# Kernel tuning notes

Measured on AMD Instinct MI355X. Metric: run time of the kernel, lower is better.

The kernel has to match this reference:

```python
import jax, jax.numpy as jnp
import numpy as np

B, T, N_EMBD, HEAD = 8, 2048, 1024, 64

def setup_inputs() -> dict:
    key = jax.random.key(0)
    k1, k2, k3, k4 = jax.random.split(key, 4)
    scale = 0.02
    return {
        "x": jax.random.normal(k1, (B, T, N_EMBD), dtype=jnp.float32),
        "Wk": jax.random.normal(k2, (N_EMBD, HEAD), dtype=jnp.float32) * scale,
        "Wq": jax.random.normal(k3, (N_EMBD, HEAD), dtype=jnp.float32) * scale,
        "Wv": jax.random.normal(k4, (N_EMBD, HEAD), dtype=jnp.float32) * scale,
    }

def reference(x, Wk, Wq, Wv):
    # x: [B, T, C]; projections are bias-free Linear(C -> head_size)
    Bx, Tx, C = x.shape
    k = x @ Wk  # [B, T, H]
    q = x @ Wq  # [B, T, H]
    v = x @ Wv  # [B, T, H]
    # NOTE: original scales by C**-0.5 with C = n_embd (not head_size)
    wei = jnp.einsum('bth,bsh->bts', q, k) * (C ** -0.5)  # [B, T, T]
    causal = jnp.tril(jnp.ones((Tx, Tx), dtype=bool))
    wei = jnp.where(causal, wei, -jnp.inf)
    wei = jax.nn.softmax(wei, axis=-1)
    out = jnp.einsum('bts,bsh->bth', wei, v)  # [B, T, H]
    return out
```

## Files before the change

kernel.cpp:

```cpp
#include <hip/hip_runtime.h>
#include <math.h>

#define B_ 8
#define T_ 2048
#define C_ 1024
#define H_ 64

typedef __attribute__((ext_vector_type(8))) short bf16x8;
typedef __attribute__((ext_vector_type(4))) float f32x4;
typedef __attribute__((ext_vector_type(16))) float f32x16;
typedef __attribute__((ext_vector_type(4))) unsigned u32x4;
typedef __attribute__((ext_vector_type(2))) unsigned u32x2;

static __device__ __forceinline__ short f2bf(float f) {
    unsigned u = __float_as_uint(f);
    unsigned r = (u + 0x7FFFu + ((u >> 16) & 1u)) >> 16;
    return (short)r;
}

static __device__ __forceinline__ unsigned cvt_pk_bf16(float lo, float hi) {
    unsigned r;
    asm("v_cvt_pk_bf16_f32 %0, %1, %2" : "=v"(r) : "v"(lo), "v"(hi));
    return r;
}

static __device__ __forceinline__ u32x2 p32(unsigned a, unsigned b) {
    return __builtin_amdgcn_permlane32_swap(a, b, false, false);
}
static __device__ __forceinline__ float xmax32(float x) {
    u32x2 r = p32(__float_as_uint(x), __float_as_uint(x));
    return fmaxf(__uint_as_float(r[0]), __uint_as_float(r[1]));
}
static __device__ __forceinline__ float xsum32(float x) {
    u32x2 r = p32(__float_as_uint(x), __float_as_uint(x));
    return __uint_as_float(r[0]) + __uint_as_float(r[1]);
}


__global__ __launch_bounds__(256) void wtrans_kernel(
    const float* __restrict__ Wq, const float* __restrict__ Wk,
    const float* __restrict__ Wv, short* __restrict__ WT)
{
    const int n  = blockIdx.x;
    const int k0 = threadIdx.x * 4;
    const float* Wsel = (n < 64) ? Wq : (n < 128 ? Wk : Wv);
    const int h = n & 63;
    short4 pk;
    pk.x = f2bf(Wsel[(size_t)(k0 + 0) * H_ + h]);
    pk.y = f2bf(Wsel[(size_t)(k0 + 1) * H_ + h]);
    pk.z = f2bf(Wsel[(size_t)(k0 + 2) * H_ + h]);
    pk.w = f2bf(Wsel[(size_t)(k0 + 3) * H_ + h]);
    *reinterpret_cast<short4*>(&WT[(size_t)n * C_ + k0]) = pk;
}

__global__ __launch_bounds__(256) void proj_kernel(
    const float* __restrict__ x, const short* __restrict__ WT,
    short* __restrict__ qF, short* __restrict__ kF, short* __restrict__ vF)
{
    __shared__ short Xs[32][72];
    __shared__ short Ws[192][72];

    const int tid  = threadIdx.x;
    const int m0   = blockIdx.x * 32;
    const int w    = tid >> 6;
    const int rs   = w >> 1;
    const int ch   = w & 1;
    const int lane = tid & 63;
    const int col  = lane & 15;
    const int g    = lane >> 4;

    const int srow = tid >> 3;
    const int sk0  = (tid & 7) * 8;
    const float* xs_src = &x[(size_t)(m0 + srow) * C_ + sk0];

    int wrow[6], wc8[6];
#pragma unroll
    for (int t6 = 0; t6 < 6; ++t6) {
        int idx = tid + t6 * 256;
        wrow[t6] = idx >> 3;
        wc8[t6]  = (idx & 7) * 8;
    }

    f32x4 acc[6];
#pragma unroll
    for (int nt = 0; nt < 6; ++nt) acc[nt] = (f32x4){0.f, 0.f, 0.f, 0.f};

    float4 xa0 = *reinterpret_cast<const float4*>(xs_src);
    float4 xb0 = *reinterpret_cast<const float4*>(xs_src + 4);
    float4 xa1 = *reinterpret_cast<const float4*>(xs_src + 64);
    float4 xb1 = *reinterpret_cast<const float4*>(xs_src + 68);
    bf16x8 wr[6];
#pragma unroll
    for (int t6 = 0; t6 < 6; ++t6)
        wr[t6] = *reinterpret_cast<const bf16x8*>(&WT[(size_t)wrow[t6] * C_ + wc8[t6]]);

#define PROJ_STEP(KB, XA, XB)                                                  \
    {                                                                          \
        __syncthreads();                                                       \
        u32x4 xw;                                                              \
        xw[0] = cvt_pk_bf16((XA).x, (XA).y);                                   \
        xw[1] = cvt_pk_bf16((XA).z, (XA).w);                                   \
        xw[2] = cvt_pk_bf16((XB).x, (XB).y);                                   \
        xw[3] = cvt_pk_bf16((XB).z, (XB).w);                                   \
        *reinterpret_cast<u32x4*>(&Xs[srow][sk0]) = xw;                        \
        _Pragma("unroll")                                                      \
        for (int t6 = 0; t6 < 6; ++t6)                                         \
            *reinterpret_cast<bf16x8*>(&Ws[wrow[t6]][wc8[t6]]) = wr[t6];       \
        __syncthreads();                                                       \
        if ((KB) + 128 < C_) {                                                 \
            XA = *reinterpret_cast<const float4*>(xs_src + (KB) + 128);        \
            XB = *reinterpret_cast<const float4*>(xs_src + (KB) + 132);        \
        }                                                                      \
        if ((KB) + 64 < C_) {                                                  \
            _Pragma("unroll")                                                  \
            for (int t6 = 0; t6 < 6; ++t6)                                     \
                wr[t6] = *reinterpret_cast<const bf16x8*>(                     \
                    &WT[(size_t)wrow[t6] * C_ + (KB) + 64 + wc8[t6]]);         \
        }                                                                      \
        bf16x8 a0 = *reinterpret_cast<const bf16x8*>(&Xs[rs * 16 + col][g * 8]);      \
        bf16x8 a1 = *reinterpret_cast<const bf16x8*>(&Xs[rs * 16 + col][32 + g * 8]); \
        _Pragma("unroll")                                                      \
        for (int nt = 0; nt < 6; ++nt) {                                       \
            const int ng = ch * 6 + nt;                                        \
            bf16x8 b0 = *reinterpret_cast<const bf16x8*>(&Ws[ng * 16 + col][g * 8]);      \
            bf16x8 b1 = *reinterpret_cast<const bf16x8*>(&Ws[ng * 16 + col][32 + g * 8]); \
            acc[nt] = __builtin_amdgcn_mfma_f32_16x16x32_bf16(a0, b0, acc[nt], 0, 0, 0);  \
            acc[nt] = __builtin_amdgcn_mfma_f32_16x16x32_bf16(a1, b1, acc[nt], 0, 0, 0);  \
        }                                                                      \
    }

    for (int s2 = 0; s2 < 8; ++s2) {
        const int kb = s2 * 128;
        PROJ_STEP(kb, xa0, xb0);
        PROJ_STEP(kb + 64, xa1, xb1);
    }
#undef PROJ_STEP

    const int trow0 = m0 + rs * 16 + g * 4;
    const int bb    = trow0 >> 11;
    const int tloc  = trow0 & 2047;
    const size_t base = (size_t)bb * T_ * H_;
    const int hiq = col >> 3, eq = col & 7;
#pragma unroll
    for (int nt = 0; nt < 6; ++nt) {
        const int ng = ch * 6 + nt;
        if (ng < 4) {
#pragma unroll
            for (int r = 0; r < 4; ++r) {
                const int tl  = tloc + r;
                const int jq  = tl >> 5, lnq = tl & 31;
                qF[base + (size_t)(((jq * 4 + ng) * 64) + hiq * 32 + lnq) * 8 + eq]
                    = f2bf(acc[nt][r]);
            }
        } else if (ng < 8) {
#pragma unroll
            for (int r = 0; r < 4; ++r) {
                const int tl   = tloc + r;
                const int kb2  = tl >> 6, half = (tl >> 5) & 1, lnk = tl & 31;
                kF[base + (size_t)((((kb2 * 2 + half) * 4 + (ng - 4)) * 64)
                                   + hiq * 32 + lnk) * 8 + eq]
                    = f2bf(acc[nt][r]);
            }
        } else {
            const int kb2 = tloc >> 6, kt = (tloc >> 4) & 3;
            const int vhi = (tloc >> 3) & 1, e0 = tloc & 7;
            const int h   = (ng - 8) * 16 + col;
            const int hs  = h >> 5, vln = h & 31;
            short4 pk;
            pk.x = f2bf(acc[nt][0]); pk.y = f2bf(acc[nt][1]);
            pk.z = f2bf(acc[nt][2]); pk.w = f2bf(acc[nt][3]);
            *reinterpret_cast<short4*>(
                &vF[base + (size_t)((((kb2 * 2 + hs) * 4 + kt) * 64)
                                    + vhi * 32 + vln) * 8 + e0]) = pk;
        }
    }
}

__global__ __launch_bounds__(512) void attn_kernel(
    const short* __restrict__ qF, const short* __restrict__ kF,
    const short* __restrict__ vF, float* __restrict__ out)
{
    __shared__ float Ob[8][32][68];
    __shared__ float Ml[8][32][2];

    const int tid  = threadIdx.x;
    const int w    = tid >> 6;
    const int lane = tid & 63;
    const int ln   = lane & 31;
    const int hi   = lane >> 5;
    const int bid  = blockIdx.x;
    const int b    = bid & 7;
    const int j    = 63 - (bid >> 3);
    const int qt0  = j * 32;
    const int n64  = (j >> 1) + 1;

    const size_t base = (size_t)b * T_ * H_;
    const short* qFb = qF + base;
    const short* kFb = kF + base;
    const short* vFb = vF + base;

    bf16x8 qf[4];
#pragma unroll
    for (int ht = 0; ht < 4; ++ht)
        qf[ht] = *reinterpret_cast<const bf16x8*>(
            &qFb[(size_t)((j * 4 + ht) * 64 + lane) * 8]);

    float m_i = -INFINITY, l_i = 0.f;
    f32x16 acc0, acc1;
#pragma unroll
    for (int r = 0; r < 16; ++r) { acc0[r] = 0.f; acc1[r] = 0.f; }

    for (int kb = w; kb < n64; kb += 8) {
        const short* kblk = &kFb[(size_t)kb * 4096];
        const short* vblk = &vFb[(size_t)kb * 4096];

        f32x16 s0, s1;
#pragma unroll
        for (int r = 0; r < 16; ++r) { s0[r] = 0.f; s1[r] = 0.f; }
#pragma unroll
        for (int ht = 0; ht < 4; ++ht) {
            bf16x8 ka0 = *reinterpret_cast<const bf16x8*>(
                &kblk[(size_t)((ht * 64) + lane) * 8]);
            bf16x8 ka1 = *reinterpret_cast<const bf16x8*>(
                &kblk[(size_t)(((4 + ht) * 64) + lane) * 8]);
            s0 = __builtin_amdgcn_mfma_f32_32x32x16_bf16(ka0, qf[ht], s0, 0, 0, 0);
            s1 = __builtin_amdgcn_mfma_f32_32x32x16_bf16(ka1, qf[ht], s1, 0, 0, 0);
        }

        bf16x8 va0[4];
#pragma unroll
        for (int kt = 0; kt < 4; ++kt)
            va0[kt] = *reinterpret_cast<const bf16x8*>(
                &vblk[(size_t)((kt * 64) + lane) * 8]);

#pragma unroll
        for (int r = 0; r < 16; ++r) { s0[r] *= 0.03125f; s1[r] *= 0.03125f; }
        if (kb == n64 - 1) {
            const int qglob = qt0 + ln;
            const int kb0   = kb * 64 + hi * 4;
#pragma unroll
            for (int r = 0; r < 16; ++r) {
                const int key = kb0 + (r & 3) + 8 * (r >> 2);
                if (key > qglob)      s0[r] = -INFINITY;
                if (key + 32 > qglob) s1[r] = -INFINITY;
            }
        }

        float t8[8];
#pragma unroll
        for (int r = 0; r < 8; ++r)
            t8[r] = fmaxf(fmaxf(s0[r], s0[r + 8]), fmaxf(s1[r], s1[r + 8]));
#pragma unroll
        for (int r = 0; r < 4; ++r) t8[r] = fmaxf(t8[r], t8[r + 4]);
        float mx = fmaxf(fmaxf(t8[0], t8[2]), fmaxf(t8[1], t8[3]));
        mx = xmax32(mx);

        const float mn    = fmaxf(m_i, mx);
        const float alpha = __expf(m_i - mn);
        m_i = mn;

#pragma unroll
        for (int r = 0; r < 16; ++r) {
            s0[r] = __expf(s0[r] - mn);
            s1[r] = __expf(s1[r] - mn);
        }
#pragma unroll
        for (int r = 0; r < 8; ++r)
            t8[r] = (s0[r] + s0[r + 8]) + (s1[r] + s1[r + 8]);
#pragma unroll
        for (int r = 0; r < 4; ++r) t8[r] = t8[r] + t8[r + 4];
        float ls = (t8[0] + t8[2]) + (t8[1] + t8[3]);
        ls = xsum32(ls);
        l_i = l_i * alpha + ls;

#pragma unroll
        for (int r = 0; r < 16; ++r) { acc0[r] *= alpha; acc1[r] *= alpha; }

        unsigned W0 = cvt_pk_bf16(s0[0],  s0[1]);
        unsigned W1 = cvt_pk_bf16(s0[2],  s0[3]);
        unsigned W2 = cvt_pk_bf16(s0[4],  s0[5]);
        unsigned W3 = cvt_pk_bf16(s0[6],  s0[7]);
        unsigned W4 = cvt_pk_bf16(s0[8],  s0[9]);
        unsigned W5 = cvt_pk_bf16(s0[10], s0[11]);
        unsigned W6 = cvt_pk_bf16(s0[12], s0[13]);
        unsigned W7 = cvt_pk_bf16(s0[14], s0[15]);
        u32x2 ra = p32(W0, W2), rb = p32(W1, W3);
        u32x4 bw0 = (u32x4){ra[0], rb[0], ra[1], rb[1]};
        ra = p32(W4, W6); rb = p32(W5, W7);
        u32x4 bw1 = (u32x4){ra[0], rb[0], ra[1], rb[1]};
        W0 = cvt_pk_bf16(s1[0],  s1[1]);
        W1 = cvt_pk_bf16(s1[2],  s1[3]);
        W2 = cvt_pk_bf16(s1[4],  s1[5]);
        W3 = cvt_pk_bf16(s1[6],  s1[7]);
        W4 = cvt_pk_bf16(s1[8],  s1[9]);
        W5 = cvt_pk_bf16(s1[10], s1[11]);
        W6 = cvt_pk_bf16(s1[12], s1[13]);
        W7 = cvt_pk_bf16(s1[14], s1[15]);
        ra = p32(W0, W2); rb = p32(W1, W3);
        u32x4 bw2 = (u32x4){ra[0], rb[0], ra[1], rb[1]};
        ra = p32(W4, W6); rb = p32(W5, W7);
        u32x4 bw3 = (u32x4){ra[0], rb[0], ra[1], rb[1]};
        bf16x8 pb0 = *reinterpret_cast<bf16x8*>(&bw0);
        bf16x8 pb1 = *reinterpret_cast<bf16x8*>(&bw1);
        bf16x8 pb2 = *reinterpret_cast<bf16x8*>(&bw2);
        bf16x8 pb3 = *reinterpret_cast<bf16x8*>(&bw3);

        bf16x8 va1[4];
#pragma unroll
        for (int kt = 0; kt < 4; ++kt)
            va1[kt] = *reinterpret_cast<const bf16x8*>(
                &vblk[(size_t)(((4 + kt) * 64) + lane) * 8]);

        acc0 = __builtin_amdgcn_mfma_f32_32x32x16_bf16(va0[0], pb0, acc0, 0, 0, 0);
        acc0 = __builtin_amdgcn_mfma_f32_32x32x16_bf16(va0[1], pb1, acc0, 0, 0, 0);
        acc0 = __builtin_amdgcn_mfma_f32_32x32x16_bf16(va0[2], pb2, acc0, 0, 0, 0);
        acc0 = __builtin_amdgcn_mfma_f32_32x32x16_bf16(va0[3], pb3, acc0, 0, 0, 0);
        acc1 = __builtin_amdgcn_mfma_f32_32x32x16_bf16(va1[0], pb0, acc1, 0, 0, 0);
        acc1 = __builtin_amdgcn_mfma_f32_32x32x16_bf16(va1[1], pb1, acc1, 0, 0, 0);
        acc1 = __builtin_amdgcn_mfma_f32_32x32x16_bf16(va1[2], pb2, acc1, 0, 0, 0);
        acc1 = __builtin_amdgcn_mfma_f32_32x32x16_bf16(va1[3], pb3, acc1, 0, 0, 0);
    }

#pragma unroll
    for (int part = 0; part < 4; ++part) {
        f32x4 v0 = (f32x4){acc0[part*4+0], acc0[part*4+1], acc0[part*4+2], acc0[part*4+3]};
        f32x4 v1 = (f32x4){acc1[part*4+0], acc1[part*4+1], acc1[part*4+2], acc1[part*4+3]};
        *reinterpret_cast<f32x4*>(&Ob[w][ln][hi * 4 + part * 8])      = v0;
        *reinterpret_cast<f32x4*>(&Ob[w][ln][32 + hi * 4 + part * 8]) = v1;
    }
    if (hi == 0) {
        Ml[w][ln][0] = m_i;
        Ml[w][ln][1] = l_i;
    }
    __syncthreads();

    float ms = -INFINITY;
#pragma unroll
    for (int w2 = 0; w2 < 8; ++w2) ms = fmaxf(ms, Ml[w2][ln][0]);
    float lsum = 0.f;
    float o[4];
#pragma unroll
    for (int e = 0; e < 4; ++e) o[e] = 0.f;
    const int h0 = w * 8 + hi * 4;
#pragma unroll
    for (int w2 = 0; w2 < 8; ++w2) {
        const float a = __expf(Ml[w2][ln][0] - ms);
        lsum += Ml[w2][ln][1] * a;
        const float* ob = &Ob[w2][ln][h0];
#pragma unroll
        for (int e = 0; e < 4; ++e) o[e] += a * ob[e];
    }
    const float inv = 1.f / lsum;
    f32x4 r0 = (f32x4){o[0] * inv, o[1] * inv, o[2] * inv, o[3] * inv};
    *reinterpret_cast<f32x4*>(&out[base + (size_t)(qt0 + ln) * H_ + h0]) = r0;
}

extern "C" void kernel_launch(void* const* d_in, const int* in_sizes, int n_in,
                              void* d_out, int out_size, void* d_ws, size_t ws_size,
                              hipStream_t stream)
{
    const float* x  = (const float*)d_in[0];
    const float* Wk = (const float*)d_in[1];
    const float* Wq = (const float*)d_in[2];
    const float* Wv = (const float*)d_in[3];
    float* out = (float*)d_out;

    short* WT = (short*)d_ws;
    short* qF = WT + (size_t)192 * C_;
    short* kF = qF + (size_t)B_ * T_ * H_;
    short* vF = kF + (size_t)B_ * T_ * H_;

    wtrans_kernel<<<dim3(192), 256, 0, stream>>>(Wq, Wk, Wv, WT);
    proj_kernel<<<dim3((B_ * T_) / 32), 256, 0, stream>>>(x, WT, qF, kF, vF);
    attn_kernel<<<dim3(T_ / 32 * B_), 512, 0, stream>>>(qF, kF, vF, out);
}
```

Measured before the change: 40.60 us.

## Process two 32-row query tiles per block to reuse K/V loads

```diff
diff --git a/kernel.cpp b/kernel.cpp
--- a/kernel.cpp
+++ b/kernel.cpp
@@ -190,120 +190,136 @@
     const int hi   = lane >> 5;
     const int bid  = blockIdx.x;
     const int b    = bid & 7;
-    const int j    = 63 - (bid >> 3);
-    const int qt0  = j * 32;
-    const int n64  = (j >> 1) + 1;
+    const int j64  = 31 - (bid >> 3);
+    const int qt0  = j64 * 64;
+    const int nkb  = j64 + 1;
 
     const size_t base = (size_t)b * T_ * H_;
     const short* qFb = qF + base;
     const short* kFb = kF + base;
     const short* vFb = vF + base;
 
-    bf16x8 qf[4];
-#pragma unroll
-    for (int ht = 0; ht < 4; ++ht)
-        qf[ht] = *reinterpret_cast<const bf16x8*>(
-            &qFb[(size_t)((j * 4 + ht) * 64 + lane) * 8]);
-
-    float m_i = -INFINITY, l_i = 0.f;
-    f32x16 acc0, acc1;
-#pragma unroll
-    for (int r = 0; r < 16; ++r) { acc0[r] = 0.f; acc1[r] = 0.f; }
-
-    for (int kb = w; kb < n64; kb += 8) {
+    bf16x8 qfA[4], qfB[4];
+#pragma unroll
+    for (int ht = 0; ht < 4; ++ht) {
+        qfA[ht] = *reinterpret_cast<const bf16x8*>(
+            &qFb[(size_t)(((2 * j64) * 4 + ht) * 64 + lane) * 8]);
+        qfB[ht] = *reinterpret_cast<const bf16x8*>(
+            &qFb[(size_t)(((2 * j64 + 1) * 4 + ht) * 64 + lane) * 8]);
+    }
+
+    float mA = -INFINITY, lA = 0.f, mB = -INFINITY, lB = 0.f;
+    f32x16 accA0, accA1, accB0, accB1;
+#pragma unroll
+    for (int r = 0; r < 16; ++r) {
+        accA0[r] = 0.f; accA1[r] = 0.f; accB0[r] = 0.f; accB1[r] = 0.f;
+    }
+
+    for (int kb = w; kb < nkb; kb += 8) {
         const short* kblk = &kFb[(size_t)kb * 4096];
         const short* vblk = &vFb[(size_t)kb * 4096];
+        const bool last = (kb == nkb - 1);
+        const int kb0 = kb * 64 + hi * 4;
+
+        bf16x8 ka0[4], ka1[4];
+#pragma unroll
+        for (int ht = 0; ht < 4; ++ht) {
+            ka0[ht] = *reinterpret_cast<const bf16x8*>(&kblk[(size_t)((ht * 64) + lane) * 8]);
+            ka1[ht] = *reinterpret_cast<const bf16x8*>(&kblk[(size_t)(((4 + ht) * 64) + lane) * 8]);
+        }
 
         f32x16 s0, s1;
 #pragma unroll
         for (int r = 0; r < 16; ++r) { s0[r] = 0.f; s1[r] = 0.f; }
 #pragma unroll
         for (int ht = 0; ht < 4; ++ht) {
-            bf16x8 ka0 = *reinterpret_cast<const bf16x8*>(
-                &kblk[(size_t)((ht * 64) + lane) * 8]);
-            bf16x8 ka1 = *reinterpret_cast<const bf16x8*>(
-                &kblk[(size_t)(((4 + ht) * 64) + lane) * 8]);
-            s0 = __builtin_amdgcn_mfma_f32_32x32x16_bf16(ka0, qf[ht], s0, 0, 0, 0);
-            s1 = __builtin_amdgcn_mfma_f32_32x32x16_bf16(ka1, qf[ht], s1, 0, 0, 0);
+            s0 = __builtin_amdgcn_mfma_f32_32x32x16_bf16(ka0[ht], qfA[ht], s0, 0, 0, 0);
+            s1 = __builtin_amdgcn_mfma_f32_32x32x16_bf16(ka1[ht], qfA[ht], s1, 0, 0, 0);
         }
 
         bf16x8 va0[4];
 #pragma unroll
         for (int kt = 0; kt < 4; ++kt)
-            va0[kt] = *reinterpret_cast<const bf16x8*>(
-                &vblk[(size_t)((kt * 64) + lane) * 8]);
+            va0[kt] = *reinterpret_cast<const bf16x8*>(&vblk[(size_t)((kt * 64) + lane) * 8]);
 
 #pragma unroll
         for (int r = 0; r < 16; ++r) { s0[r] *= 0.03125f; s1[r] *= 0.03125f; }
-        if (kb == n64 - 1) {
-            const int qglob = qt0 + ln;
-            const int kb0   = kb * 64 + hi * 4;
+        if (last) {
+            const int qg = qt0 + ln;
 #pragma unroll
             for (int r = 0; r < 16; ++r) {
                 const int key = kb0 + (r & 3) + 8 * (r >> 2);
-                if (key > qglob)      s0[r] = -INFINITY;
-                if (key + 32 > qglob) s1[r] = -INFINITY;
+                if (key > qg)      s0[r] = -INFINITY;
+                if (key + 32 > qg) s1[r] = -INFINITY;
             }
         }
-
-        float t8[8];
-#pragma unroll
-        for (int r = 0; r < 8; ++r)
-            t8[r] = fmaxf(fmaxf(s0[r], s0[r + 8]), fmaxf(s1[r], s1[r + 8]));
-#pragma unroll
-        for (int r = 0; r < 4; ++r) t8[r] = fmaxf(t8[r], t8[r + 4]);
-        float mx = fmaxf(fmaxf(t8[0], t8[2]), fmaxf(t8[1], t8[3]));
-        mx = xmax32(mx);
-
-        const float mn    = fmaxf(m_i, mx);
-        const float alpha = __expf(m_i - mn);
-        m_i = mn;
-
-#pragma unroll
-        for (int r = 0; r < 16; ++r) {
-            s0[r] = __expf(s0[r] - mn);
-            s1[r] = __expf(s1[r] - mn);
-        }
-#pragma unroll
-        for (int r = 0; r < 8; ++r)
-            t8[r] = (s0[r] + s0[r + 8]) + (s1[r] + s1[r + 8]);
-#pragma unroll
-        for (int r = 0; r < 4; ++r) t8[r] = t8[r] + t8[r + 4];
-        float ls = (t8[0] + t8[2]) + (t8[1] + t8[3]);
-        ls = xsum32(ls);
-        l_i = l_i * alpha + ls;
-
-#pragma unroll
-        for (int r = 0; r < 16; ++r) { acc0[r] *= alpha; acc1[r] *= alpha; }
-
-        unsigned W0 = cvt_pk_bf16(s0[0],  s0[1]);
-        unsigned W1 = cvt_pk_bf16(s0[2],  s0[3]);
-        unsigned W2 = cvt_pk_bf16(s0[4],  s0[5]);
-        unsigned W3 = cvt_pk_bf16(s0[6],  s0[7]);
-        unsigned W4 = cvt_pk_bf16(s0[8],  s0[9]);
-        unsigned W5 = cvt_pk_bf16(s0[10], s0[11]);
-        unsigned W6 = cvt_pk_bf16(s0[12], s0[13]);
-        unsigned W7 = cvt_pk_bf16(s0[14], s0[15]);
-        u32x2 ra = p32(W0, W2), rb = p32(W1, W3);
-        u32x4 bw0 = (u32x4){ra[0], rb[0], ra[1], rb[1]};
-        ra = p32(W4, W6); rb = p32(W5, W7);
-        u32x4 bw1 = (u32x4){ra[0], rb[0], ra[1], rb[1]};
-        W0 = cvt_pk_bf16(s1[0],  s1[1]);
-        W1 = cvt_pk_bf16(s1[2],  s1[3]);
-        W2 = cvt_pk_bf16(s1[4],  s1[5]);
-        W3 = cvt_pk_bf16(s1[6],  s1[7]);
-        W4 = cvt_pk_bf16(s1[8],  s1[9]);
-        W5 = cvt_pk_bf16(s1[10], s1[11]);
-        W6 = cvt_pk_bf16(s1[12], s1[13]);
-        W7 = cvt_pk_bf16(s1[14], s1[15]);
-        ra = p32(W0, W2); rb = p32(W1, W3);
-        u32x4 bw2 = (u32x4){ra[0], rb[0], ra[1], rb[1]};
-        ra = p32(W4, W6); rb = p32(W5, W7);
-        u32x4 bw3 = (u32x4){ra[0], rb[0], ra[1], rb[1]};
-        bf16x8 pb0 = *reinterpret_cast<bf16x8*>(&bw0);
-        bf16x8 pb1 = *reinterpret_cast<bf16x8*>(&bw1);
-        bf16x8 pb2 = *reinterpret_cast<bf16x8*>(&bw2);
-        bf16x8 pb3 = *reinterpret_cast<bf16x8*>(&bw3);
+        {
+            float t8[8];
+#pragma unroll
+            for (int r = 0; r < 8; ++r)
+                t8[r] = fmaxf(fmaxf(s0[r], s0[r + 8]), fmaxf(s1[r], s1[r + 8]));
+#pragma unroll
+            for (int r = 0; r < 4; ++r) t8[r] = fmaxf(t8[r], t8[r + 4]);
+            float mx = fmaxf(fmaxf(t8[0], t8[2]), fmaxf(t8[1], t8[3]));
+            mx = xmax32(mx);
+            const float mn    = fmaxf(mA, mx);
+            const float alpha = __expf(mA - mn);
+            mA = mn;
+#pragma unroll
+            for (int r = 0; r < 16; ++r) {
+                s0[r] = __expf(s0[r] - mn);
+                s1[r] = __expf(s1[r] - mn);
+            }
+#pragma unroll
+            for (int r = 0; r < 8; ++r)
+                t8[r] = (s0[r] + s0[r + 8]) + (s1[r] + s1[r + 8]);
+#pragma unroll
+            for (int r = 0; r < 4; ++r) t8[r] = t8[r] + t8[r + 4];
+            float ls = (t8[0] + t8[2]) + (t8[1] + t8[3]);
+            ls = xsum32(ls);
+            lA = lA * alpha + ls;
+#pragma unroll
+            for (int r = 0; r < 16; ++r) { accA0[r] *= alpha; accA1[r] *= alpha; }
+        }
+        bf16x8 pbA0, pbA1, pbA2, pbA3;
+        {
+            unsigned W0 = cvt_pk_bf16(s0[0],  s0[1]);
+            unsigned W1 = cvt_pk_bf16(s0[2],  s0[3]);
+            unsigned W2 = cvt_pk_bf16(s0[4],  s0[5]);
+            unsigned W3 = cvt_pk_bf16(s0[6],  s0[7]);
+            unsigned W4 = cvt_pk_bf16(s0[8],  s0[9]);
+            unsigned W5 = cvt_pk_bf16(s0[10], s0[11]);
+            unsigned W6 = cvt_pk_bf16(s0[12], s0[13]);
+            unsigned W7 = cvt_pk_bf16(s0[14], s0[15]);
+            u32x2 ra = p32(W0, W2), rb = p32(W1, W3);
+            u32x4 bw0 = (u32x4){ra[0], rb[0], ra[1], rb[1]};
+            ra = p32(W4, W6); rb = p32(W5, W7);
+            u32x4 bw1 = (u32x4){ra[0], rb[0], ra[1], rb[1]};
+            W0 = cvt_pk_bf16(s1[0],  s1[1]);
+            W1 = cvt_pk_bf16(s1[2],  s1[3]);
+            W2 = cvt_pk_bf16(s1[4],  s1[5]);
+            W3 = cvt_pk_bf16(s1[6],  s1[7]);
+            W4 = cvt_pk_bf16(s1[8],  s1[9]);
+            W5 = cvt_pk_bf16(s1[10], s1[11]);
+            W6 = cvt_pk_bf16(s1[12], s1[13]);
+            W7 = cvt_pk_bf16(s1[14], s1[15]);
+            ra = p32(W0, W2); rb = p32(W1, W3);
+            u32x4 bw2 = (u32x4){ra[0], rb[0], ra[1], rb[1]};
+            ra = p32(W4, W6); rb = p32(W5, W7);
+            u32x4 bw3 = (u32x4){ra[0], rb[0], ra[1], rb[1]};
+            pbA0 = *reinterpret_cast<bf16x8*>(&bw0);
+            pbA1 = *reinterpret_cast<bf16x8*>(&bw1);
+            pbA2 = *reinterpret_cast<bf16x8*>(&bw2);
+            pbA3 = *reinterpret_cast<bf16x8*>(&bw3);
+        }
+
+#pragma unroll
+        for (int r = 0; r < 16; ++r) { s0[r] = 0.f; s1[r] = 0.f; }
+#pragma unroll
+        for (int ht = 0; ht < 4; ++ht) {
+            s0 = __builtin_amdgcn_mfma_f32_32x32x16_bf16(ka0[ht], qfB[ht], s0, 0, 0, 0);
+            s1 = __builtin_amdgcn_mfma_f32_32x32x16_bf16(ka1[ht], qfB[ht], s1, 0, 0, 0);
+        }
 
         bf16x8 va1[4];
 #pragma unroll
@@ -311,48 +327,158 @@
             va1[kt] = *reinterpret_cast<const bf16x8*>(
                 &vblk[(size_t)(((4 + kt) * 64) + lane) * 8]);
 
-        acc0 = __builtin_amdgcn_mfma_f32_32x32x16_bf16(va0[0], pb0, acc0, 0, 0, 0);
-        acc0 = __builtin_amdgcn_mfma_f32_32x32x16_bf16(va0[1], pb1, acc0, 0, 0, 0);
-        acc0 = __builtin_amdgcn_mfma_f32_32x32x16_bf16(va0[2], pb2, acc0, 0, 0, 0);
-        acc0 = __builtin_amdgcn_mfma_f32_32x32x16_bf16(va0[3], pb3, acc0, 0, 0, 0);
-        acc1 = __builtin_amdgcn_mfma_f32_32x32x16_bf16(va1[0], pb0, acc1, 0, 0, 0);
-        acc1 = __builtin_amdgcn_mfma_f32_32x32x16_bf16(va1[1], pb1, acc1, 0, 0, 0);
-        acc1 = __builtin_amdgcn_mfma_f32_32x32x16_bf16(va1[2], pb2, acc1, 0, 0, 0);
-        acc1 = __builtin_amdgcn_mfma_f32_32x32x16_bf16(va1[3], pb3, acc1, 0, 0, 0);
-    }
+#pragma unroll
+        for (int r = 0; r < 16; ++r) { s0[r] *= 0.03125f; s1[r] *= 0.03125f; }
+        if (last) {
+            const int qg = qt0 + 32 + ln;
+#pragma unroll
+            for (int r = 0; r < 16; ++r) {
+                const int key = kb0 + (r & 3) + 8 * (r >> 2);
+                if (key > qg)      s0[r] = -INFINITY;
+                if (key + 32 > qg) s1[r] = -INFINITY;
+            }
+        }
+        {
+            float t8[8];
+#pragma unroll
+            for (int r = 0; r < 8; ++r)
+                t8[r] = fmaxf(fmaxf(s0[r], s0[r + 8]), fmaxf(s1[r], s1[r + 8]));
+#pragma unroll
+            for (int r = 0; r < 4; ++r) t8[r] = fmaxf(t8[r], t8[r + 4]);
+            float mx = fmaxf(fmaxf(t8[0], t8[2]), fmaxf(t8[1], t8[3]));
+            mx = xmax32(mx);
+            const float mn    = fmaxf(mB, mx);
+            const float alpha = __expf(mB - mn);
+            mB = mn;
+#pragma unroll
+            for (int r = 0; r < 16; ++r) {
+                s0[r] = __expf(s0[r] - mn);
+                s1[r] = __expf(s1[r] - mn);
+            }
+            float u8[8];
+#pragma unroll
+            for (int r = 0; r < 8; ++r)
+                u8[r] = (s0[r] + s0[r + 8]) + (s1[r] + s1[r + 8]);
+#pragma unroll
+            for (int r = 0; r < 4; ++r) u8[r] = u8[r] + u8[r + 4];
+            float ls = (u8[0] + u8[2]) + (u8[1] + u8[3]);
+            ls = xsum32(ls);
+            lB = lB * alpha + ls;
+#pragma unroll
+            for (int r = 0; r < 16; ++r) { accB0[r] *= alpha; accB1[r] *= alpha; }
+        }
+        bf16x8 pbB0, pbB1, pbB2, pbB3;
+        {
+            unsigned W0 = cvt_pk_bf16(s0[0],  s0[1]);
+            unsigned W1 = cvt_pk_bf16(s0[2],  s0[3]);
+            unsigned W2 = cvt_pk_bf16(s0[4],  s0[5]);
+            unsigned W3 = cvt_pk_bf16(s0[6],  s0[7]);
+            unsigned W4 = cvt_pk_bf16(s0[8],  s0[9]);
+            unsigned W5 = cvt_pk_bf16(s0[10], s0[11]);
+            unsigned W6 = cvt_pk_bf16(s0[12], s0[13]);
+            unsigned W7 = cvt_pk_bf16(s0[14], s0[15]);
+            u32x2 ra = p32(W0, W2), rb = p32(W1, W3);
+            u32x4 bw0 = (u32x4){ra[0], rb[0], ra[1], rb[1]};
+            ra = p32(W4, W6); rb = p32(W5, W7);
+            u32x4 bw1 = (u32x4){ra[0], rb[0], ra[1], rb[1]};
+            W0 = cvt_pk_bf16(s1[0],  s1[1]);
+            W1 = cvt_pk_bf16(s1[2],  s1[3]);
+            W2 = cvt_pk_bf16(s1[4],  s1[5]);
+            W3 = cvt_pk_bf16(s1[6],  s1[7]);
+            W4 = cvt_pk_bf16(s1[8],  s1[9]);
+            W5 = cvt_pk_bf16(s1[10], s1[11]);
+            W6 = cvt_pk_bf16(s1[12], s1[13]);
+            W7 = cvt_pk_bf16(s1[14], s1[15]);
+            ra = p32(W0, W2); rb = p32(W1, W3);
+            u32x4 bw2 = (u32x4){ra[0], rb[0], ra[1], rb[1]};
+            ra = p32(W4, W6); rb = p32(W5, W7);
+            u32x4 bw3 = (u32x4){ra[0], rb[0], ra[1], rb[1]};
+            pbB0 = *reinterpret_cast<bf16x8*>(&bw0);
+            pbB1 = *reinterpret_cast<bf16x8*>(&bw1);
+            pbB2 = *reinterpret_cast<bf16x8*>(&bw2);
+            pbB3 = *reinterpret_cast<bf16x8*>(&bw3);
+        }
+
+        accA0 = __builtin_amdgcn_mfma_f32_32x32x16_bf16(va0[0], pbA0, accA0, 0, 0, 0);
+        accA0 = __builtin_amdgcn_mfma_f32_32x32x16_bf16(va0[1], pbA1, accA0, 0, 0, 0);
+        accA0 = __builtin_amdgcn_mfma_f32_32x32x16_bf16(va0[2], pbA2, accA0, 0, 0, 0);
+        accA0 = __builtin_amdgcn_mfma_f32_32x32x16_bf16(va0[3], pbA3, accA0, 0, 0, 0);
+        accA1 = __builtin_amdgcn_mfma_f32_32x32x16_bf16(va1[0], pbA0, accA1, 0, 0, 0);
+        accA1 = __builtin_amdgcn_mfma_f32_32x32x16_bf16(va1[1], pbA1, accA1, 0, 0, 0);
+        accA1 = __builtin_amdgcn_mfma_f32_32x32x16_bf16(va1[2], pbA2, accA1, 0, 0, 0);
+        accA1 = __builtin_amdgcn_mfma_f32_32x32x16_bf16(va1[3], pbA3, accA1, 0, 0, 0);
+        accB0 = __builtin_amdgcn_mfma_f32_32x32x16_bf16(va0[0], pbB0, accB0, 0, 0, 0);
+        accB0 = __builtin_amdgcn_mfma_f32_32x32x16_bf16(va0[1], pbB1, accB0, 0, 0, 0);
+        accB0 = __builtin_amdgcn_mfma_f32_32x32x16_bf16(va0[2], pbB2, accB0, 0, 0, 0);
+        accB0 = __builtin_amdgcn_mfma_f32_32x32x16_bf16(va0[3], pbB3, accB0, 0, 0, 0);
+        accB1 = __builtin_amdgcn_mfma_f32_32x32x16_bf16(va1[0], pbB0, accB1, 0, 0, 0);
+        accB1 = __builtin_amdgcn_mfma_f32_32x32x16_bf16(va1[1], pbB1, accB1, 0, 0, 0);
+        accB1 = __builtin_amdgcn_mfma_f32_32x32x16_bf16(va1[2], pbB2, accB1, 0, 0, 0);
+        accB1 = __builtin_amdgcn_mfma_f32_32x32x16_bf16(va1[3], pbB3, accB1, 0, 0, 0);
+    }
+
+    const int h0 = w * 8 + hi * 4;
 
 #pragma unroll
     for (int part = 0; part < 4; ++part) {
-        f32x4 v0 = (f32x4){acc0[part*4+0], acc0[part*4+1], acc0[part*4+2], acc0[part*4+3]};
-        f32x4 v1 = (f32x4){acc1[part*4+0], acc1[part*4+1], acc1[part*4+2], acc1[part*4+3]};
+        f32x4 v0 = (f32x4){accA0[part*4+0], accA0[part*4+1], accA0[part*4+2], accA0[part*4+3]};
+        f32x4 v1 = (f32x4){accA1[part*4+0], accA1[part*4+1], accA1[part*4+2], accA1[part*4+3]};
         *reinterpret_cast<f32x4*>(&Ob[w][ln][hi * 4 + part * 8])      = v0;
         *reinterpret_cast<f32x4*>(&Ob[w][ln][32 + hi * 4 + part * 8]) = v1;
     }
-    if (hi == 0) {
-        Ml[w][ln][0] = m_i;
-        Ml[w][ln][1] = l_i;
-    }
+    if (hi == 0) { Ml[w][ln][0] = mA; Ml[w][ln][1] = lA; }
     __syncthreads();
-
-    float ms = -INFINITY;
-#pragma unroll
-    for (int w2 = 0; w2 < 8; ++w2) ms = fmaxf(ms, Ml[w2][ln][0]);
-    float lsum = 0.f;
-    float o[4];
-#pragma unroll
-    for (int e = 0; e < 4; ++e) o[e] = 0.f;
-    const int h0 = w * 8 + hi * 4;
-#pragma unroll
-    for (int w2 = 0; w2 < 8; ++w2) {
-        const float a = __expf(Ml[w2][ln][0] - ms);
-        lsum += Ml[w2][ln][1] * a;
-        const float* ob = &Ob[w2][ln][h0];
-#pragma unroll
-        for (int e = 0; e < 4; ++e) o[e] += a * ob[e];
-    }
-    const float inv = 1.f / lsum;
-    f32x4 r0 = (f32x4){o[0] * inv, o[1] * inv, o[2] * inv, o[3] * inv};
-    *reinterpret_cast<f32x4*>(&out[base + (size_t)(qt0 + ln) * H_ + h0]) = r0;
+    {
+        float ms = -INFINITY;
+#pragma unroll
+        for (int w2 = 0; w2 < 8; ++w2) ms = fmaxf(ms, Ml[w2][ln][0]);
+        float lsum = 0.f;
+        float o[4];
+#pragma unroll
+        for (int e = 0; e < 4; ++e) o[e] = 0.f;
+#pragma unroll
+        for (int w2 = 0; w2 < 8; ++w2) {
+            const float a = __expf(Ml[w2][ln][0] - ms);
+            lsum += Ml[w2][ln][1] * a;
+            const float* ob = &Ob[w2][ln][h0];
+#pragma unroll
+            for (int e = 0; e < 4; ++e) o[e] += a * ob[e];
+        }
+        const float inv = 1.f / lsum;
+        f32x4 r0 = (f32x4){o[0] * inv, o[1] * inv, o[2] * inv, o[3] * inv};
+        *reinterpret_cast<f32x4*>(&out[base + (size_t)(qt0 + ln) * H_ + h0]) = r0;
+    }
+    __syncthreads();
+
+#pragma unroll
+    for (int part = 0; part < 4; ++part) {
+        f32x4 v0 = (f32x4){accB0[part*4+0], accB0[part*4+1], accB0[part*4+2], accB0[part*4+3]};
+        f32x4 v1 = (f32x4){accB1[part*4+0], accB1[part*4+1], accB1[part*4+2], accB1[part*4+3]};
+        *reinterpret_cast<f32x4*>(&Ob[w][ln][hi * 4 + part * 8])      = v0;
+        *reinterpret_cast<f32x4*>(&Ob[w][ln][32 + hi * 4 + part * 8]) = v1;
+    }
+    if (hi == 0) { Ml[w][ln][0] = mB; Ml[w][ln][1] = lB; }
+    __syncthreads();
+    {
+        float ms = -INFINITY;
+#pragma unroll
+        for (int w2 = 0; w2 < 8; ++w2) ms = fmaxf(ms, Ml[w2][ln][0]);
+        float lsum = 0.f;
+        float o[4];
+#pragma unroll
+        for (int e = 0; e < 4; ++e) o[e] = 0.f;
+#pragma unroll
+        for (int w2 = 0; w2 < 8; ++w2) {
+            const float a = __expf(Ml[w2][ln][0] - ms);
+            lsum += Ml[w2][ln][1] * a;
+            const float* ob = &Ob[w2][ln][h0];
+#pragma unroll
+            for (int e = 0; e < 4; ++e) o[e] += a * ob[e];
+        }
+        const float inv = 1.f / lsum;
+        f32x4 r0 = (f32x4){o[0] * inv, o[1] * inv, o[2] * inv, o[3] * inv};
+        *reinterpret_cast<f32x4*>(&out[base + (size_t)(qt0 + 32 + ln) * H_ + h0]) = r0;
+    }
 }
 
 extern "C" void kernel_launch(void* const* d_in, const int* in_sizes, int n_in,
@@ -372,5 +498,5 @@
 
     wtrans_kernel<<<dim3(192), 256, 0, stream>>>(Wq, Wk, Wv, WT);
     proj_kernel<<<dim3((B_ * T_) / 32), 256, 0, stream>>>(x, WT, qF, kF, vF);
-    attn_kernel<<<dim3(T_ / 32 * B_), 512, 0, stream>>>(qF, kF, vF, out);
-}
+    attn_kernel<<<dim3(T_ / 64 * B_), 512, 0, stream>>>(qF, kF, vF, out);
+}
```

Result: slower. 44.40 us (+9.4%).

## Stage projection outputs through shared memory and deepen x prefetch

Applied to the files above, without the earlier changes.

```diff
diff --git a/kernel.cpp b/kernel.cpp
--- a/kernel.cpp
+++ b/kernel.cpp
@@ -59,6 +59,7 @@
 {
     __shared__ short Xs[32][72];
     __shared__ short Ws[192][72];
+    __shared__ short St[3][2048];
 
     const int tid  = threadIdx.x;
     const int m0   = blockIdx.x * 32;
@@ -85,10 +86,14 @@
 #pragma unroll
     for (int nt = 0; nt < 6; ++nt) acc[nt] = (f32x4){0.f, 0.f, 0.f, 0.f};
 
-    float4 xa0 = *reinterpret_cast<const float4*>(xs_src);
-    float4 xb0 = *reinterpret_cast<const float4*>(xs_src + 4);
-    float4 xa1 = *reinterpret_cast<const float4*>(xs_src + 64);
-    float4 xb1 = *reinterpret_cast<const float4*>(xs_src + 68);
+    float4 xA0 = *reinterpret_cast<const float4*>(xs_src);
+    float4 xB0 = *reinterpret_cast<const float4*>(xs_src + 4);
+    float4 xA1 = *reinterpret_cast<const float4*>(xs_src + 64);
+    float4 xB1 = *reinterpret_cast<const float4*>(xs_src + 68);
+    float4 xA2 = *reinterpret_cast<const float4*>(xs_src + 128);
+    float4 xB2 = *reinterpret_cast<const float4*>(xs_src + 132);
+    float4 xA3 = *reinterpret_cast<const float4*>(xs_src + 192);
+    float4 xB3 = *reinterpret_cast<const float4*>(xs_src + 196);
     bf16x8 wr[6];
 #pragma unroll
     for (int t6 = 0; t6 < 6; ++t6)
@@ -107,11 +112,11 @@
         for (int t6 = 0; t6 < 6; ++t6)                                         \
             *reinterpret_cast<bf16x8*>(&Ws[wrow[t6]][wc8[t6]]) = wr[t6];       \
         __syncthreads();                                                       \
-        if ((KB) + 128 < C_) {                                                 \
-            XA = *reinterpret_cast<const float4*>(xs_src + (KB) + 128);        \
-            XB = *reinterpret_cast<const float4*>(xs_src + (KB) + 132);        \
+        if ((KB) + 256 < C_) {                   \
+            XA = *reinterpret_cast<const float4*>(xs_src + (KB) + 256);        \
+            XB = *reinterpret_cast<const float4*>(xs_src + (KB) + 260);        \
         }                                                                      \
-        if ((KB) + 64 < C_) {                                                  \
+        if ((KB) + 64 < C_) {                     \
             _Pragma("unroll")                                                  \
             for (int t6 = 0; t6 < 6; ++t6)                                     \
                 wr[t6] = *reinterpret_cast<const bf16x8*>(                     \
@@ -129,50 +134,61 @@
         }                                                                      \
     }
 
-    for (int s2 = 0; s2 < 8; ++s2) {
-        const int kb = s2 * 128;
-        PROJ_STEP(kb, xa0, xb0);
-        PROJ_STEP(kb + 64, xa1, xb1);
+    for (int s4 = 0; s4 < 4; ++s4) {
+        const int kb = s4 * 256;
+        PROJ_STEP(kb,       xA0, xB0);
+        PROJ_STEP(kb + 64,  xA1, xB1);
+        PROJ_STEP(kb + 128, xA2, xB2);
+        PROJ_STEP(kb + 192, xA3, xB3);
     }
 #undef PROJ_STEP
 
-    const int trow0 = m0 + rs * 16 + g * 4;
-    const int bb    = trow0 >> 11;
-    const int tloc  = trow0 & 2047;
-    const size_t base = (size_t)bb * T_ * H_;
-    const int hiq = col >> 3, eq = col & 7;
+    const int tl2b = rs * 16 + g * 4;
+    const int hiq  = col >> 3, eq = col & 7;
 #pragma unroll
     for (int nt = 0; nt < 6; ++nt) {
         const int ng = ch * 6 + nt;
         if (ng < 4) {
 #pragma unroll
-            for (int r = 0; r < 4; ++r) {
-                const int tl  = tloc + r;
-                const int jq  = tl >> 5, lnq = tl & 31;
-                qF[base + (size_t)(((jq * 4 + ng) * 64) + hiq * 32 + lnq) * 8 + eq]
-                    = f2bf(acc[nt][r]);
-            }
+            for (int r = 0; r < 4; ++r)
+                St[0][((ng * 64) + hiq * 32 + tl2b + r) * 8 + eq] = f2bf(acc[nt][r]);
         } else if (ng < 8) {
 #pragma unroll
-            for (int r = 0; r < 4; ++r) {
-                const int tl   = tloc + r;
-                const int kb2  = tl >> 6, half = (tl >> 5) & 1, lnk = tl & 31;
-                kF[base + (size_t)((((kb2 * 2 + half) * 4 + (ng - 4)) * 64)
-                                   + hiq * 32 + lnk) * 8 + eq]
-                    = f2bf(acc[nt][r]);
-            }
+            for (int r = 0; r < 4; ++r)
+                St[1][(((ng - 4) * 64) + hiq * 32 + tl2b + r) * 8 + eq] = f2bf(acc[nt][r]);
         } else {
-            const int kb2 = tloc >> 6, kt = (tloc >> 4) & 3;
-            const int vhi = (tloc >> 3) & 1, e0 = tloc & 7;
             const int h   = (ng - 8) * 16 + col;
             const int hs  = h >> 5, vln = h & 31;
+            const int c   = hs * 2 + ((tl2b >> 4) & 1);
+            const int vhi = (tl2b >> 3) & 1, e0 = tl2b & 7;
             short4 pk;
             pk.x = f2bf(acc[nt][0]); pk.y = f2bf(acc[nt][1]);
             pk.z = f2bf(acc[nt][2]); pk.w = f2bf(acc[nt][3]);
             *reinterpret_cast<short4*>(
-                &vF[base + (size_t)((((kb2 * 2 + hs) * 4 + kt) * 64)
-                                    + vhi * 32 + vln) * 8 + e0]) = pk;
+                &St[2][c * 512 + (vhi * 32 + vln) * 8 + e0]) = pk;
         }
+    }
+    __syncthreads();
+
+    const int    mloc  = m0 & 2047;
+    const size_t base  = (size_t)(m0 >> 11) * T_ * H_;
+    {
+        const size_t qbase = base + (size_t)((mloc >> 5) * 4) * 512;
+        *reinterpret_cast<bf16x8*>(&qF[qbase + tid * 8]) =
+            *reinterpret_cast<const bf16x8*>(&St[0][tid * 8]);
+    }
+    {
+        const int kb2 = mloc >> 6, half = (mloc >> 5) & 1;
+        const size_t kbase = base + (size_t)((kb2 * 2 + half) * 4) * 512;
+        *reinterpret_cast<bf16x8*>(&kF[kbase + tid * 8]) =
+            *reinterpret_cast<const bf16x8*>(&St[1][tid * 8]);
+    }
+    {
+        const int kb2 = mloc >> 6, kt0 = (mloc >> 4) & 3;
+        const int c = tid >> 6, hs = c >> 1, kt = kt0 + (c & 1);
+        const size_t vbase = base + (size_t)((kb2 * 2 + hs) * 4 + kt) * 512;
+        *reinterpret_cast<bf16x8*>(&vF[vbase + (tid & 63) * 8]) =
+            *reinterpret_cast<const bf16x8*>(&St[2][tid * 8]);
     }
 }
 
```

Result: slower. 42.09 us (+3.7%).
